# Performance work log

Measured on AMD Instinct MI355X. Metric: run time of the kernel, lower is better.

The kernel has to match this reference:

```python
import jax, jax.numpy as jnp
import numpy as np

HEADS = 16
KV_HEADS = 4
HEAD_DIM = 64
HIDDEN = 1024
ROPE_THETA = 10000.0
NEG = -1e9


def _rope_cos_sin(seq_len, head_dim, dtype):
    inv_freq = 1.0 / (ROPE_THETA ** (jnp.arange(0, head_dim, 2, dtype=jnp.float32) / head_dim))
    pos = jnp.arange(seq_len, dtype=jnp.float32)
    freqs = jnp.outer(pos, inv_freq)                      # [S, d/2]
    emb = jnp.concatenate([freqs, freqs], axis=-1)        # [S, d]
    return jnp.cos(emb).astype(dtype), jnp.sin(emb).astype(dtype)


def _rotate_half(x):
    x1, x2 = jnp.split(x, 2, axis=-1)
    return jnp.concatenate([-x2, x1], axis=-1)


def setup_inputs() -> dict:
    key = jax.random.key(0)
    ks = jax.random.split(key, 5)
    B, S = 2, 2048
    hidden_states = jax.random.normal(ks[0], (B, S, HIDDEN), dtype=jnp.float32)
    # additive causal mask [1,1,S,S]
    causal = jnp.tril(jnp.ones((S, S), dtype=bool))
    attention_mask = jnp.where(causal, 0.0, NEG).astype(jnp.float32)[None, None]
    scale = 0.02
    Wq = jax.random.normal(ks[1], (HIDDEN, HEADS * HEAD_DIM), dtype=jnp.float32) * scale
    Wk = jax.random.normal(ks[2], (HIDDEN, KV_HEADS * HEAD_DIM), dtype=jnp.float32) * scale
    Wv = jax.random.normal(ks[3], (HIDDEN, KV_HEADS * HEAD_DIM), dtype=jnp.float32) * scale
    Wo = jax.random.normal(ks[4], (HEADS * HEAD_DIM, HIDDEN), dtype=jnp.float32) * scale
    return {"hidden_states": hidden_states, "attention_mask": attention_mask,
            "Wq": Wq, "Wk": Wk, "Wv": Wv, "Wo": Wo}


def reference(hidden_states, attention_mask, Wq, Wk, Wv, Wo):
    B, S, _ = hidden_states.shape
    G = HEADS // KV_HEADS  # kv groups

    q = (hidden_states @ Wq).reshape(B, S, HEADS, HEAD_DIM).transpose(0, 2, 1, 3)      # [B,H,S,d]
    k = (hidden_states @ Wk).reshape(B, S, KV_HEADS, HEAD_DIM).transpose(0, 2, 1, 3)   # [B,Hk,S,d]
    v = (hidden_states @ Wv).reshape(B, S, KV_HEADS, HEAD_DIM).transpose(0, 2, 1, 3)   # [B,Hk,S,d]

    cos, sin = _rope_cos_sin(S, HEAD_DIM, q.dtype)  # [S,d], broadcasts over B,H
    q = q * cos + _rotate_half(q) * sin
    k = k * cos + _rotate_half(k) * sin

    # GQA: query head h attends to kv head h // G (== repeat_interleave on kv heads)
    qg = q.reshape(B, KV_HEADS, G, S, HEAD_DIM)
    scores = jnp.einsum('bkgqd,bkld->bkgql', qg, k) / np.float32(np.sqrt(HEAD_DIM))  # [B,Hk,G,S,S]
    scores = scores + attention_mask[:, :, None, :, :]
    probs = jax.nn.softmax(scores.astype(jnp.float32), axis=-1).astype(q.dtype)
    out = jnp.einsum('bkgql,bkld->bkgqd', probs, v)            # [B,Hk,G,S,d]
    out = out.reshape(B, HEADS, S, HEAD_DIM).transpose(0, 2, 1, 3).reshape(B, S, HEADS * HEAD_DIM)
    return out @ Wo
```

## Files before the change

kernel.cpp:

```cpp
#include <hip/hip_runtime.h>
#include <hip/hip_bf16.h>
#include <math.h>

#define HEADS 16
#define KV_HEADS 4
#define HEAD_DIM 64
#define HIDDEN 1024
#define BATCH 2
#define SEQ 2048
#define ROWS (BATCH*SEQ)
#define NQKV (HEADS*HEAD_DIM + 2*KV_HEADS*HEAD_DIM)
#define QSCL 0.1803368867f

typedef float f32x4 __attribute__((ext_vector_type(4)));
typedef __bf16 bf16x8 __attribute__((ext_vector_type(8)));
typedef int int4v __attribute__((ext_vector_type(4)));

static __device__ __forceinline__ unsigned short f2bf(float f) {
    union { float f; unsigned int u; } v; v.f = f;
    unsigned int r = v.u + 0x7fffu + ((v.u >> 16) & 1u);
    return (unsigned short)(r >> 16);
}

#define GLOAD_LDS16(gaddr, laddr) \
    __builtin_amdgcn_global_load_lds( \
        (const __attribute__((address_space(1))) unsigned int*)(gaddr), \
        (__attribute__((address_space(3))) unsigned int*)(laddr), 16, 0, 0)

__global__ __launch_bounds__(256) void k_fprep(const float* __restrict__ hs,
                                               const float* __restrict__ Wq,
                                               const float* __restrict__ Wk,
                                               const float* __restrict__ Wv,
                                               const float* __restrict__ Wo,
                                               unsigned short* __restrict__ hsb,
                                               unsigned short* __restrict__ WqkvT,
                                               unsigned short* __restrict__ WoT,
                                               float* __restrict__ cosT,
                                               float* __restrict__ sinT) {
    __shared__ float tile[64][65];
    int bx = blockIdx.x;
    if (bx < 640) {
        const float* src; unsigned short* dst; int ld, n0, k0;
        if (bx < 384) {
            int tn = bx % 24, tk = bx / 24;
            n0 = tn * 64; k0 = tk * 64; dst = WqkvT;
            if (n0 < 1024)      { src = Wq + n0;          ld = 1024; }
            else if (n0 < 1280) { src = Wk + (n0 - 1024); ld = 256;  }
            else                { src = Wv + (n0 - 1280); ld = 256;  }
        } else {
            int i2 = bx - 384;
            int tn = i2 & 15, tk = i2 >> 4;
            n0 = tn * 64; k0 = tk * 64;
            src = Wo + n0; ld = 1024; dst = WoT;
        }
        int tx = threadIdx.x & 63, ty = threadIdx.x >> 6;
#pragma unroll
        for (int j = 0; j < 16; j++) {
            int k = j * 4 + ty;
            tile[k][tx] = src[(size_t)(k0 + k) * ld + tx];
        }
        __syncthreads();
#pragma unroll
        for (int j = 0; j < 16; j++) {
            int r = j * 4 + ty;
            dst[(size_t)(n0 + r) * 1024 + k0 + tx] = f2bf(tile[tx][r]);
        }
    } else {
        int idx = (bx - 640) * 256 + threadIdx.x;
        int stride = 384 * 256;
        for (int i = idx; i < ROWS * HIDDEN / 4; i += stride) {
            float4 v = ((const float4*)hs)[i];
            hsb[i*4+0] = f2bf(v.x); hsb[i*4+1] = f2bf(v.y);
            hsb[i*4+2] = f2bf(v.z); hsb[i*4+3] = f2bf(v.w);
        }
        for (int i = idx; i < SEQ * 32; i += stride) {
            int s = i >> 5, f = i & 31;
            float inv = powf(10000.0f, -(float)f / 32.0f);
            float ang = (float)s * inv;
            cosT[i] = cosf(ang); sinT[i] = sinf(ang);
        }
    }
}

template <bool BF16_OUT, bool ROPE>
__global__ __launch_bounds__(256) void k_gemm(const unsigned short* __restrict__ A,
                                              const unsigned short* __restrict__ Bt,
                                              void* __restrict__ Cv,
                                              const float* __restrict__ cosT,
                                              const float* __restrict__ sinT,
                                              int M, int N, int K) {
    __shared__ unsigned short lA[128*64];
    __shared__ unsigned short lB[128*64];
    const int tid = threadIdx.x;
    const int lane = tid & 63;
    const int wid = tid >> 6;
    const int wr = wid >> 1, wc = wid & 1;
    const int m0 = blockIdx.y * 128;
    const int n0 = blockIdx.x * 128;
    const int l15 = lane & 15, lq = lane >> 4;

    f32x4 acc[4][4];
#pragma unroll
    for (int i = 0; i < 4; i++)
#pragma unroll
        for (int j = 0; j < 4; j++) acc[i][j] = (f32x4){0.f,0.f,0.f,0.f};

    for (int k0 = 0; k0 < K; k0 += 64) {
        __syncthreads();
#pragma unroll
        for (int it = 0; it < 4; ++it) {
            int c = tid + it * 256;
            int row = c >> 3, slot = c & 7;
            int gs = slot ^ (row & 7);
            GLOAD_LDS16(A + (size_t)(m0 + row) * K + k0 + gs * 8, (char*)lA + c * 16);
            GLOAD_LDS16(Bt + (size_t)(n0 + row) * K + k0 + gs * 8, (char*)lB + c * 16);
        }
        __syncthreads();
#pragma unroll
        for (int t = 0; t < 2; t++) {
            bf16x8 af[4], bfr[4];
#pragma unroll
            for (int i = 0; i < 4; i++) {
                int row = wr * 64 + i * 16 + l15;
                int slot = (t * 4 + lq) ^ (row & 7);
                af[i] = *(const bf16x8*)((const char*)lA + row * 128 + slot * 16);
            }
#pragma unroll
            for (int j = 0; j < 4; j++) {
                int row = wc * 64 + j * 16 + l15;
                int slot = (t * 4 + lq) ^ (row & 7);
                bfr[j] = *(const bf16x8*)((const char*)lB + row * 128 + slot * 16);
            }
#pragma unroll
            for (int i = 0; i < 4; i++)
#pragma unroll
                for (int j = 0; j < 4; j++)
                    acc[i][j] = __builtin_amdgcn_mfma_f32_16x16x32_bf16(af[i], bfr[j], acc[i][j], 0, 0, 0);
        }
    }
    if constexpr (ROPE) {
        const int hc0 = n0 + wc * 64;
        if (hc0 < 1280) {
            const float scl = (hc0 < 1024) ? QSCL : 1.0f;
#pragma unroll
            for (int i = 0; i < 4; i++) {
#pragma unroll
                for (int r = 0; r < 4; r++) {
                    int row = m0 + wr * 64 + i * 16 + lq * 4 + r;
                    int s = row & (SEQ - 1);
                    float c_lo = cosT[s * 32 + l15],      c_hi = cosT[s * 32 + 16 + l15];
                    float s_lo = sinT[s * 32 + l15],      s_hi = sinT[s * 32 + 16 + l15];
#pragma unroll
                    for (int j = 0; j < 4; j++) {
                        float c  = (j & 1) ? c_hi : c_lo;
                        float sn = (j & 1) ? s_hi : s_lo;
                        float v = acc[i][j][r], vp = acc[i][j ^ 2][r];
                        float o = (j < 2) ? (v * c - vp * sn) : (v * c + vp * sn);
                        int col = n0 + wc * 64 + j * 16 + l15;
                        ((unsigned short*)Cv)[(size_t)row * N + col] = f2bf(o * scl);
                    }
                }
            }
            return;
        }
    }
#pragma unroll
    for (int i = 0; i < 4; i++) {
#pragma unroll
        for (int j = 0; j < 4; j++) {
            int col = n0 + wc * 64 + j * 16 + l15;
#pragma unroll
            for (int r = 0; r < 4; r++) {
                int row = m0 + wr * 64 + i * 16 + lq * 4 + r;
                if constexpr (BF16_OUT)
                    ((unsigned short*)Cv)[(size_t)row * N + col] = f2bf(acc[i][j][r]);
                else
                    ((float*)Cv)[(size_t)row * N + col] = acc[i][j][r];
            }
        }
    }
}

__global__ __launch_bounds__(256) void k_vtrans(const unsigned short* __restrict__ QKVb,
                                                unsigned short* __restrict__ Vt) {
    __shared__ unsigned short tile[64][66];
    int s0 = blockIdx.x * 64;
    int bhk = blockIdx.y;
    int b = bhk >> 2, hk = bhk & 3;
    int t = threadIdx.x;
    int r = t >> 3, c = t & 7;
    const unsigned short* base = QKVb + (size_t)b * SEQ * NQKV + 1280 + hk * 64;
#pragma unroll
    for (int rr = r; rr < 64; rr += 32) {
        unsigned short tmp[8];
        *(int4v*)tmp = *(const int4v*)(base + (size_t)(s0 + rr) * NQKV + c * 8);
#pragma unroll
        for (int e = 0; e < 8; e++) tile[rr][c * 8 + e] = tmp[e];
    }
    __syncthreads();
    unsigned short* outb = Vt + (size_t)bhk * 64 * SEQ;
#pragma unroll
    for (int dd = r; dd < 64; dd += 32) {
        unsigned short tmp[8];
#pragma unroll
        for (int e = 0; e < 8; e++) tmp[e] = tile[c * 8 + e][dd];
        *(int4v*)(outb + (size_t)dd * SEQ + s0 + c * 8) = *(int4v*)tmp;
    }
}

__global__ __launch_bounds__(256) void k_attn(const unsigned short* __restrict__ QKVb,
                                              const unsigned short* __restrict__ Vt,
                                              unsigned short* __restrict__ Ob) {
    __shared__ unsigned short lK[2][64*64];
    __shared__ unsigned short lV[2][64*64];
    __shared__ unsigned short lP[4][16*64];
    const int tid = threadIdx.x;
    const int lane = tid & 63;
    const int w = tid >> 6;
    const int l15 = lane & 15, lq = lane >> 4;
    const int bh = blockIdx.x;
    const int qt = (int)gridDim.y - 1 - (int)blockIdx.y;
    const int b = bh >> 4, h = bh & 15;
    const int hk = h >> 2;
    const int q0 = qt * 64;

    bf16x8 aq[2];
    {
        int s = q0 + w * 16 + l15;
        const unsigned short* Qp = QKVb + (size_t)(b * SEQ + s) * NQKV + h * 64;
        aq[0] = *(const bf16x8*)(Qp + lq * 8);
        aq[1] = *(const bf16x8*)(Qp + 32 + lq * 8);
    }

    f32x4 oacc[4];
    float mrun[4], lrun[4];
#pragma unroll
    for (int d = 0; d < 4; d++) {
        oacc[d] = (f32x4){0.f,0.f,0.f,0.f};
        mrun[d] = -INFINITY; lrun[d] = 0.f;
    }

    const unsigned short* Kg = QKVb + (size_t)b * SEQ * NQKV + 1024 + hk * 64;
    const unsigned short* Vg = Vt + (size_t)(b * KV_HEADS + hk) * 64 * SEQ;

#define STAGE_KV(buf, kv0)                                                        \
    {                                                                             \
        _Pragma("unroll")                                                         \
        for (int it = 0; it < 2; ++it) {                                          \
            int c = tid + it * 256;                                               \
            int row = c >> 3, slot = c & 7;                                       \
            int gs = slot ^ (row & 7);                                            \
            GLOAD_LDS16(Kg + (size_t)((kv0) + row) * NQKV + gs * 8,               \
                        (char*)lK[buf] + c * 16);                                 \
            GLOAD_LDS16(Vg + (size_t)row * SEQ + (kv0) + gs * 8,                  \
                        (char*)lV[buf] + c * 16);                                 \
        }                                                                         \
    }

    STAGE_KV(0, 0);
    __syncthreads();
    int cur = 0;

    for (int j = 0; j <= qt; ++j) {
        if (j < qt) STAGE_KV(cur ^ 1, (j + 1) * 64);

        int kv0 = j * 64;
        f32x4 sf[4];
#pragma unroll
        for (int kb = 0; kb < 4; kb++) {
            sf[kb] = (f32x4){0.f,0.f,0.f,0.f};
#pragma unroll
            for (int t = 0; t < 2; t++) {
                int row = kb * 16 + l15;
                int slot = (t * 4 + lq) ^ (row & 7);
                bf16x8 bk = *(const bf16x8*)((const char*)lK[cur] + row * 128 + slot * 16);
                sf[kb] = __builtin_amdgcn_mfma_f32_16x16x32_bf16(aq[t], bk, sf[kb], 0, 0, 0);
            }
        }
        if (j == qt) {
#pragma unroll
            for (int kb = 0; kb < 4; kb++)
#pragma unroll
                for (int r = 0; r < 4; r++) {
                    int kv = kv0 + kb * 16 + l15;
                    int q = q0 + w * 16 + lq * 4 + r;
                    if (kv > q) sf[kb][r] = -INFINITY;
                }
        }
#pragma unroll
        for (int r = 0; r < 4; r++) {
            float m = fmaxf(fmaxf(sf[0][r], sf[1][r]), fmaxf(sf[2][r], sf[3][r]));
            m = fmaxf(m, __shfl_xor(m, 1));
            m = fmaxf(m, __shfl_xor(m, 2));
            m = fmaxf(m, __shfl_xor(m, 4));
            m = fmaxf(m, __shfl_xor(m, 8));
            if (__any(m > mrun[r])) {
                float newm = fmaxf(mrun[r], m);
                float fac = exp2f(mrun[r] - newm);
                mrun[r] = newm;
                lrun[r] *= fac;
#pragma unroll
                for (int d = 0; d < 4; d++) oacc[d][r] *= fac;
            }
            float rs = 0.f;
#pragma unroll
            for (int kb = 0; kb < 4; kb++) {
                float p = exp2f(sf[kb][r] - mrun[r]);
                sf[kb][r] = p; rs += p;
            }
            rs += __shfl_xor(rs, 1); rs += __shfl_xor(rs, 2);
            rs += __shfl_xor(rs, 4); rs += __shfl_xor(rs, 8);
            lrun[r] += rs;
        }
        unsigned short* lPw = lP[w];
#pragma unroll
        for (int kb = 0; kb < 4; kb++)
#pragma unroll
            for (int r = 0; r < 4; r++) {
                int q = lq * 4 + r;
                int kv = kb * 16 + l15;
                int byte = (q * 128 + kv * 2) ^ ((q & 7) << 4);
                *(__bf16*)((char*)lPw + byte) = (__bf16)sf[kb][r];
            }
#pragma unroll
        for (int t = 0; t < 2; t++) {
            int qr = l15;
            int slota = (t * 4 + lq) ^ (qr & 7);
            bf16x8 ap = *(const bf16x8*)((const char*)lPw + qr * 128 + slota * 16);
#pragma unroll
            for (int db = 0; db < 4; db++) {
                int vrow = db * 16 + l15;
                int slotv = (t * 4 + lq) ^ (vrow & 7);
                bf16x8 bv = *(const bf16x8*)((const char*)lV[cur] + vrow * 128 + slotv * 16);
                oacc[db] = __builtin_amdgcn_mfma_f32_16x16x32_bf16(ap, bv, oacc[db], 0, 0, 0);
            }
        }
        __syncthreads();
        cur ^= 1;
    }
    float linv[4];
#pragma unroll
    for (int r = 0; r < 4; r++) linv[r] = 1.0f / lrun[r];
#pragma unroll
    for (int db = 0; db < 4; db++)
#pragma unroll
        for (int r = 0; r < 4; r++) {
            int q = q0 + w * 16 + lq * 4 + r;
            int col = h * 64 + db * 16 + l15;
            Ob[((size_t)b * SEQ + q) * 1024 + col] = f2bf(oacc[db][r] * linv[r]);
        }
#undef STAGE_KV
}

extern "C" void kernel_launch(void* const* d_in, const int* in_sizes, int n_in,
                              void* d_out, int out_size, void* d_ws, size_t ws_size,
                              hipStream_t stream) {
    const float* hs = (const float*)d_in[0];
    const float* Wq = (const float*)d_in[2];
    const float* Wk = (const float*)d_in[3];
    const float* Wv = (const float*)d_in[4];
    const float* Wo = (const float*)d_in[5];
    float* out = (float*)d_out;

    char* ws = (char*)d_ws;
    unsigned short* hsb   = (unsigned short*)ws; ws += (size_t)ROWS * HIDDEN * 2;
    unsigned short* WqkvT = (unsigned short*)ws; ws += (size_t)NQKV * HIDDEN * 2;
    unsigned short* WoT   = (unsigned short*)ws; ws += (size_t)HIDDEN * HIDDEN * 2;
    float* cosT = (float*)ws; ws += (size_t)SEQ * 32 * 4;
    float* sinT = (float*)ws; ws += (size_t)SEQ * 32 * 4;
    unsigned short* QKVb = (unsigned short*)ws; ws += (size_t)ROWS * NQKV * 2;
    unsigned short* Vt = (unsigned short*)ws; ws += (size_t)BATCH * KV_HEADS * 64 * SEQ * 2;
    unsigned short* Ob = (unsigned short*)ws; ws += (size_t)ROWS * HIDDEN * 2;

    k_fprep<<<1024, 256, 0, stream>>>(hs, Wq, Wk, Wv, Wo, hsb, WqkvT, WoT, cosT, sinT);

    dim3 g1(NQKV / 128, ROWS / 128);
    k_gemm<true, true><<<g1, 256, 0, stream>>>(hsb, WqkvT, QKVb, cosT, sinT, ROWS, NQKV, HIDDEN);

    k_vtrans<<<dim3(SEQ / 64, BATCH * KV_HEADS), 256, 0, stream>>>(QKVb, Vt);

    dim3 ga(BATCH * HEADS, SEQ / 64);
    k_attn<<<ga, 256, 0, stream>>>(QKVb, Vt, Ob);

    dim3 g2(HIDDEN / 128, ROWS / 128);
    k_gemm<false, false><<<g2, 256, 0, stream>>>(Ob, WoT, out, nullptr, nullptr, ROWS, HIDDEN, HIDDEN);
}
```

Measured before the change: 217.0 us.

## Double-buffer GEMM LDS tiles and transpose attention score layout

The GEMM kernel now double-buffers its A/B LDS tiles and prefetches the next K-slice before computing the current one, which drops one barrier per iteration and overlaps global loads with MFMA work. The attention kernel computes scores transposed (K as the A operand), so each lane holds one query row. Row max and sum then need only two cross-lane shuffles and a single running max/sum per lane instead of four. s_setprio hints are added around the MFMA sections. This doubles GEMM LDS use to 64KB, which may lower occupancy, and adds shuffles to broadcast per-row rescale factors.

```diff
diff --git a/kernel.cpp b/kernel.cpp
--- a/kernel.cpp
+++ b/kernel.cpp
@@ -89,8 +89,8 @@
                                               const float* __restrict__ cosT,
                                               const float* __restrict__ sinT,
                                               int M, int N, int K) {
-    __shared__ unsigned short lA[128*64];
-    __shared__ unsigned short lB[128*64];
+    __shared__ unsigned short lA[2][128*64];
+    __shared__ unsigned short lB[2][128*64];
     const int tid = threadIdx.x;
     const int lane = tid & 63;
     const int wid = tid >> 6;
@@ -105,17 +105,26 @@
 #pragma unroll
         for (int j = 0; j < 4; j++) acc[i][j] = (f32x4){0.f,0.f,0.f,0.f};
 
+#define STAGE_AB(buf, k0)                                                         \
+    {                                                                             \
+        _Pragma("unroll")                                                         \
+        for (int it = 0; it < 4; ++it) {                                          \
+            int c = tid + it * 256;                                               \
+            int row = c >> 3, slot = c & 7;                                       \
+            int gs = slot ^ (row & 7);                                            \
+            GLOAD_LDS16(A + (size_t)(m0 + row) * K + (k0) + gs * 8,               \
+                        (char*)lA[buf] + c * 16);                                 \
+            GLOAD_LDS16(Bt + (size_t)(n0 + row) * K + (k0) + gs * 8,              \
+                        (char*)lB[buf] + c * 16);                                 \
+        }                                                                         \
+    }
+
+    STAGE_AB(0, 0);
+    __syncthreads();
+    int cur = 0;
+
     for (int k0 = 0; k0 < K; k0 += 64) {
-        __syncthreads();
-#pragma unroll
-        for (int it = 0; it < 4; ++it) {
-            int c = tid + it * 256;
-            int row = c >> 3, slot = c & 7;
-            int gs = slot ^ (row & 7);
-            GLOAD_LDS16(A + (size_t)(m0 + row) * K + k0 + gs * 8, (char*)lA + c * 16);
-            GLOAD_LDS16(Bt + (size_t)(n0 + row) * K + k0 + gs * 8, (char*)lB + c * 16);
-        }
-        __syncthreads();
+        if (k0 + 64 < K) STAGE_AB(cur ^ 1, k0 + 64);
 #pragma unroll
         for (int t = 0; t < 2; t++) {
             bf16x8 af[4], bfr[4];
@@ -123,13 +132,13 @@
             for (int i = 0; i < 4; i++) {
                 int row = wr * 64 + i * 16 + l15;
                 int slot = (t * 4 + lq) ^ (row & 7);
-                af[i] = *(const bf16x8*)((const char*)lA + row * 128 + slot * 16);
+                af[i] = *(const bf16x8*)((const char*)lA[cur] + row * 128 + slot * 16);
             }
 #pragma unroll
             for (int j = 0; j < 4; j++) {
                 int row = wc * 64 + j * 16 + l15;
                 int slot = (t * 4 + lq) ^ (row & 7);
-                bfr[j] = *(const bf16x8*)((const char*)lB + row * 128 + slot * 16);
+                bfr[j] = *(const bf16x8*)((const char*)lB[cur] + row * 128 + slot * 16);
             }
 #pragma unroll
             for (int i = 0; i < 4; i++)
@@ -137,7 +146,10 @@
                 for (int j = 0; j < 4; j++)
                     acc[i][j] = __builtin_amdgcn_mfma_f32_16x16x32_bf16(af[i], bfr[j], acc[i][j], 0, 0, 0);
         }
-    }
+        __syncthreads();
+        cur ^= 1;
+    }
+#undef STAGE_AB
     if constexpr (ROPE) {
         const int hc0 = n0 + wc * 64;
         if (hc0 < 1280) {
@@ -233,12 +245,9 @@
     }
 
     f32x4 oacc[4];
-    float mrun[4], lrun[4];
-#pragma unroll
-    for (int d = 0; d < 4; d++) {
-        oacc[d] = (f32x4){0.f,0.f,0.f,0.f};
-        mrun[d] = -INFINITY; lrun[d] = 0.f;
-    }
+#pragma unroll
+    for (int d = 0; d < 4; d++) oacc[d] = (f32x4){0.f,0.f,0.f,0.f};
+    float mrun = -INFINITY, lrun = 0.f;
 
     const unsigned short* Kg = QKVb + (size_t)b * SEQ * NQKV + 1024 + hk * 64;
     const unsigned short* Vg = Vt + (size_t)(b * KV_HEADS + hk) * 64 * SEQ;
@@ -265,63 +274,75 @@
         if (j < qt) STAGE_KV(cur ^ 1, (j + 1) * 64);
 
         int kv0 = j * 64;
-        f32x4 sf[4];
+        f32x4 sT[4];
+        __builtin_amdgcn_s_setprio(1);
 #pragma unroll
         for (int kb = 0; kb < 4; kb++) {
-            sf[kb] = (f32x4){0.f,0.f,0.f,0.f};
+            sT[kb] = (f32x4){0.f,0.f,0.f,0.f};
 #pragma unroll
             for (int t = 0; t < 2; t++) {
                 int row = kb * 16 + l15;
                 int slot = (t * 4 + lq) ^ (row & 7);
                 bf16x8 bk = *(const bf16x8*)((const char*)lK[cur] + row * 128 + slot * 16);
-                sf[kb] = __builtin_amdgcn_mfma_f32_16x16x32_bf16(aq[t], bk, sf[kb], 0, 0, 0);
-            }
-        }
+                sT[kb] = __builtin_amdgcn_mfma_f32_16x16x32_bf16(bk, aq[t], sT[kb], 0, 0, 0);
+            }
+        }
+        __builtin_amdgcn_s_setprio(0);
+        const int qg = q0 + w * 16 + l15;
         if (j == qt) {
 #pragma unroll
             for (int kb = 0; kb < 4; kb++)
 #pragma unroll
                 for (int r = 0; r < 4; r++) {
-                    int kv = kv0 + kb * 16 + l15;
-                    int q = q0 + w * 16 + lq * 4 + r;
-                    if (kv > q) sf[kb][r] = -INFINITY;
+                    int kvg = kv0 + kb * 16 + lq * 4 + r;
+                    if (kvg > qg) sT[kb][r] = -INFINITY;
                 }
         }
-#pragma unroll
-        for (int r = 0; r < 4; r++) {
-            float m = fmaxf(fmaxf(sf[0][r], sf[1][r]), fmaxf(sf[2][r], sf[3][r]));
-            m = fmaxf(m, __shfl_xor(m, 1));
-            m = fmaxf(m, __shfl_xor(m, 2));
-            m = fmaxf(m, __shfl_xor(m, 4));
-            m = fmaxf(m, __shfl_xor(m, 8));
-            if (__any(m > mrun[r])) {
-                float newm = fmaxf(mrun[r], m);
-                float fac = exp2f(mrun[r] - newm);
-                mrun[r] = newm;
-                lrun[r] *= fac;
-#pragma unroll
-                for (int d = 0; d < 4; d++) oacc[d][r] *= fac;
-            }
-            float rs = 0.f;
-#pragma unroll
-            for (int kb = 0; kb < 4; kb++) {
-                float p = exp2f(sf[kb][r] - mrun[r]);
-                sf[kb][r] = p; rs += p;
-            }
-            rs += __shfl_xor(rs, 1); rs += __shfl_xor(rs, 2);
-            rs += __shfl_xor(rs, 4); rs += __shfl_xor(rs, 8);
-            lrun[r] += rs;
-        }
+        float m;
+        {
+            f32x4 mx = sT[0];
+#pragma unroll
+            for (int kb = 1; kb < 4; kb++) {
+#pragma unroll
+                for (int r = 0; r < 4; r++) mx[r] = fmaxf(mx[r], sT[kb][r]);
+            }
+            m = fmaxf(fmaxf(mx[0], mx[1]), fmaxf(mx[2], mx[3]));
+            m = fmaxf(m, __shfl_xor(m, 16));
+            m = fmaxf(m, __shfl_xor(m, 32));
+        }
+        if (__any(m > mrun)) {
+            float newm = fmaxf(mrun, m);
+            float fac = exp2f(mrun - newm);
+            mrun = newm;
+            lrun *= fac;
+#pragma unroll
+            for (int r = 0; r < 4; r++) {
+                float facr = __shfl(fac, (lane & 48) | (lq * 4 + r));
+#pragma unroll
+                for (int d = 0; d < 4; d++) oacc[d][r] *= facr;
+            }
+        }
+        float rs = 0.f;
+#pragma unroll
+        for (int kb = 0; kb < 4; kb++)
+#pragma unroll
+            for (int r = 0; r < 4; r++) {
+                float p = exp2f(sT[kb][r] - mrun);
+                sT[kb][r] = p; rs += p;
+            }
+        rs += __shfl_xor(rs, 16);
+        rs += __shfl_xor(rs, 32);
+        lrun += rs;
         unsigned short* lPw = lP[w];
 #pragma unroll
         for (int kb = 0; kb < 4; kb++)
 #pragma unroll
             for (int r = 0; r < 4; r++) {
-                int q = lq * 4 + r;
-                int kv = kb * 16 + l15;
-                int byte = (q * 128 + kv * 2) ^ ((q & 7) << 4);
-                *(__bf16*)((char*)lPw + byte) = (__bf16)sf[kb][r];
-            }
+                int kv = kb * 16 + lq * 4 + r;
+                int byte = (l15 * 128 + kv * 2) ^ ((l15 & 7) << 4);
+                *(__bf16*)((char*)lPw + byte) = (__bf16)sT[kb][r];
+            }
+        __builtin_amdgcn_s_setprio(1);
 #pragma unroll
         for (int t = 0; t < 2; t++) {
             int qr = l15;
@@ -335,19 +356,21 @@
                 oacc[db] = __builtin_amdgcn_mfma_f32_16x16x32_bf16(ap, bv, oacc[db], 0, 0, 0);
             }
         }
+        __builtin_amdgcn_s_setprio(0);
         __syncthreads();
         cur ^= 1;
     }
-    float linv[4];
-#pragma unroll
-    for (int r = 0; r < 4; r++) linv[r] = 1.0f / lrun[r];
+    float linvr[4];
+#pragma unroll
+    for (int r = 0; r < 4; r++)
+        linvr[r] = 1.0f / __shfl(lrun, (lane & 48) | (lq * 4 + r));
 #pragma unroll
     for (int db = 0; db < 4; db++)
 #pragma unroll
         for (int r = 0; r < 4; r++) {
             int q = q0 + w * 16 + lq * 4 + r;
             int col = h * 64 + db * 16 + l15;
-            Ob[((size_t)b * SEQ + q) * 1024 + col] = f2bf(oacc[db][r] * linv[r]);
+            Ob[((size_t)b * SEQ + q) * 1024 + col] = f2bf(oacc[db][r] * linvr[r]);
         }
 #undef STAGE_KV
 }
```

Result: faster. 188.6 us (-13.1%).
